# Kernel optimization log

Measured on AMD Instinct MI355X. Metric: run time of the kernel, lower is better.

Reference implementation:

```python
import jax, jax.numpy as jnp
import numpy as np

K = 3          # kernel size
K2 = K * K     # ope_channels


def setup_inputs() -> dict:
    key = jax.random.key(0)
    k1, k2, k3, k4, k5 = jax.random.split(key, 5)
    b, c, h, w = 8, 64, 128, 128
    out_c = 64
    x = jax.random.normal(k1, (b, c, h, w), dtype=jnp.float32)
    # conv weight: (in_channels, out_channels, k, k) as in the torch module
    weight = jax.random.normal(k2, (c, out_c, K, K), dtype=jnp.float32) * 0.05
    bias = jax.random.normal(k3, (out_c,), dtype=jnp.float32) * 0.05
    # operator MLP: Linear(K2 -> K2*K2); torch weight layout (out_features, in_features)
    op_w = jax.random.normal(k4, (K2 * K2, K2), dtype=jnp.float32) * 0.1
    op_b = jax.random.normal(k5, (K2 * K2,), dtype=jnp.float32) * 0.01
    return {"x": x, "weight": weight, "bias": bias, "op_w": op_w, "op_b": op_b}


def _unfold(x):
    # F.unfold(kernel=3, stride=1, pad=1) -> patches ordered (c, ki, kj)
    b, c, h, w = x.shape
    xp = jnp.pad(x, ((0, 0), (0, 0), (1, 1), (1, 1)))
    # (b, c, K2, h, w) with K2 ordered row-major over (ki, kj), matching torch
    patches = jnp.stack([xp[:, :, i:i + h, j:j + w]
                         for i in range(K) for j in range(K)], axis=2)
    return patches.transpose(0, 1, 3, 4, 2)  # (b, c, h, w, K2)


def reference(x, weight, bias, op_w, op_b):
    b, c, h, w = x.shape
    xu = _unfold(x)  # (b, c, h, w, K2)
    # per-pixel patch norm over channels -> (b, h, w, K2)
    n = jnp.sqrt(jnp.sum(xu * xu, axis=1))
    # per-pixel dynamic operator: (b, h, w, K2, K2)
    op = jnp.tanh(n @ op_w.T + op_b).reshape(b, h, w, K2, K2)
    # apply operator: bchw j , bhw jk -> bchw k
    x_op = jnp.einsum('bchwj,bhwjk->bchwk', xu, op)
    # final conv weight contraction: weight (in, out, K, K) -> (out, in, K2)
    wr = weight.reshape(c, -1, K2).transpose(1, 0, 2)
    out = jnp.einsum('bchwk,ock->bohw', x_op + xu, wr)
    return out + bias[None, :, None, None]
```

## Files before the change

### kernel.cpp

```cpp
#include <hip/hip_runtime.h>
#include <math.h>
#include <stdint.h>

#define HW   128
#define CIN  64
#define OC   64
#define TW   16
#define TH   4
#define HLW  18
#define HLH  6
#define HLN  (HLW*HLH)
#define SXR  109
#define K2   9
#define KTOT (CIN*K2)
#define SOPR 81

typedef __bf16  bf16x8 __attribute__((ext_vector_type(8)));
typedef float   f32x4  __attribute__((ext_vector_type(4)));
typedef uint32_t u32x4 __attribute__((ext_vector_type(4)));

__device__ __forceinline__ ushort f32_to_bf16_rne(float f) {
    union { float f; uint32_t u; } x; x.f = f;
    return (ushort)((x.u + 0x7FFF + ((x.u >> 16) & 1)) >> 16);
}

#define PKBF16(dst, lo, hi) \
    asm("v_cvt_pk_bf16_f32 %0, %1, %2" : "=v"(dst) : "v"(lo), "v"(hi))

__global__ void prep_weight(const float* __restrict__ w, ushort* __restrict__ wt) {
    int n = blockIdx.x * 256 + threadIdx.x;
    int o = n / KTOT;
    int r = n - o * KTOT;
    int kt = r >> 6;
    int c  = r & 63;
    wt[n] = f32_to_bf16_rne(w[(c * OC + o) * K2 + kt]);
}

__global__ __launch_bounds__(256, 2)
void dyf_main(const float* __restrict__ x,
              const float* __restrict__ bias,
              const float* __restrict__ op_w,
              const float* __restrict__ op_b,
              const ushort* __restrict__ wt,
              float* __restrict__ out)
{
    __shared__ float sx[CIN * SXR];
    __shared__ float sT[HLN];
    __shared__ float sop[64 * SOPR];

    const int tid  = threadIdx.x;
    const int lane = tid & 63;
    const int wv   = tid >> 6;
    const int b    = blockIdx.z;
    const int h0   = blockIdx.y * TH;
    const int w0   = blockIdx.x * TW;

    {
        const float* __restrict__ xb = x + (size_t)b * CIN * HW * HW;
        #pragma unroll
        for (int it = 0; it < 27; ++it) {
            int i  = tid + it * 256;
            int c  = i / HLN;
            int r  = i - c * HLN;
            int hy = r / HLW;
            int hx = r - hy * HLW;
            int gy = h0 - 1 + hy;
            int gx = w0 - 1 + hx;
            float v = 0.f;
            if ((unsigned)gy < HW && (unsigned)gx < HW)
                v = xb[c * HW * HW + gy * HW + gx];
            sx[c * SXR + r] = v;
        }
    }
    __syncthreads();

    if (tid < HLN) {
        float s = 0.f;
        #pragma unroll 16
        for (int c = 0; c < CIN; ++c) { float v = sx[c * SXR + tid]; s += v * v; }
        sT[tid] = s;
    }
    __syncthreads();

    {
        const int px = tid >> 2;
        const int q  = tid & 3;
        const int py = px >> 4, pxx = px & 15;
        float nrm[9];
        #pragma unroll
        for (int j = 0; j < 9; ++j)
            nrm[j] = sqrtf(sT[(py + j / 3) * HLW + pxx + (j % 3)]);
        const int nkt = (q == 0) ? 3 : 2;
        for (int t = 0; t < 3; ++t) {
            if (t >= nkt) break;
            const int kt = (q == 0) ? ((t == 2) ? 8 : t) : (q * 2 + t);
            #pragma unroll
            for (int j = 0; j < 9; ++j) {
                const int m = j * 9 + kt;
                float a = op_b[m];
                #pragma unroll
                for (int jj = 0; jj < 9; ++jj) a += nrm[jj] * op_w[m * 9 + jj];
                float v = tanhf(a);
                if (j == kt) v += 1.0f;
                sop[px * SOPR + m] = v;
            }
        }
    }
    __syncthreads();

    const int pxx = lane & 15;
    const int g   = lane >> 4;
    const int py  = wv;

    float opf[81];
    {
        const float* srcp = &sop[(wv * 16 + pxx) * SOPR];
        #pragma unroll
        for (int m = 0; m < 81; ++m) opf[m] = srcp[m];
    }

    u32x4 zw[18];
    #pragma unroll
    for (int chalf = 0; chalf < 2; ++chalf) {
        #pragma unroll
        for (int t = 0; t < 4; ++t) {
            const int c0 = chalf * 32 + g * 8 + 2 * t;
            float xu0[9], xu1[9];
            #pragma unroll
            for (int j = 0; j < 9; ++j) {
                const int pos = (py + j / 3) * HLW + pxx + (j % 3);
                xu0[j] = sx[c0 * SXR + pos];
                xu1[j] = sx[(c0 + 1) * SXR + pos];
            }
            #pragma unroll
            for (int kt = 0; kt < 9; ++kt) {
                float y0 = 0.f, y1 = 0.f;
                #pragma unroll
                for (int j = 0; j < 9; ++j) {
                    y0 += xu0[j] * opf[j * 9 + kt];
                    y1 += xu1[j] * opf[j * 9 + kt];
                }
                uint32_t pk;
                PKBF16(pk, y0, y1);
                zw[2 * kt + chalf][t] = pk;
            }
        }
    }

    __builtin_amdgcn_sched_barrier(0);

    {
        f32x4 acc[4];
        #pragma unroll
        for (int mr = 0; mr < 4; ++mr) acc[mr] = f32x4{0.f, 0.f, 0.f, 0.f};

        #pragma unroll
        for (int s = 0; s < 18; ++s) {
            const bf16x8 bfr = __builtin_bit_cast(bf16x8, zw[s]);
            #pragma unroll
            for (int mr = 0; mr < 4; ++mr) {
                const bf16x8 af = *reinterpret_cast<const bf16x8*>(
                    wt + (mr * 16 + pxx) * KTOT + s * 32 + g * 8);
                acc[mr] = __builtin_amdgcn_mfma_f32_16x16x32_bf16(af, bfr, acc[mr], 0, 0, 0);
            }
        }
        #pragma unroll
        for (int mr = 0; mr < 4; ++mr) {
            #pragma unroll
            for (int ii = 0; ii < 4; ++ii) {
                const int o = mr * 16 + g * 4 + ii;
                out[(((size_t)b * OC + o) * HW + (h0 + wv)) * HW + w0 + pxx]
                    = acc[mr][ii] + bias[o];
            }
        }
    }
}

extern "C" void kernel_launch(void* const* d_in, const int* in_sizes, int n_in,
                              void* d_out, int out_size, void* d_ws, size_t ws_size,
                              hipStream_t stream) {
    const float* x      = (const float*)d_in[0];
    const float* weight = (const float*)d_in[1];
    const float* bias   = (const float*)d_in[2];
    const float* op_w   = (const float*)d_in[3];
    const float* op_b   = (const float*)d_in[4];
    float*  out = (float*)d_out;
    ushort* wt  = (ushort*)d_ws;

    prep_weight<<<dim3((OC * KTOT) / 256), dim3(256), 0, stream>>>(weight, wt);

    dim3 grid(HW / TW, HW / TH, 8);
    dyf_main<<<grid, dim3(256), 0, stream>>>(x, bias, op_w, op_b, wt, out);
}
```

Before: 217.5 us.

## Pack per-pixel operator as bf16 and interleave MFMA per channel half

The 81-entry per-pixel operator is now stored in shared memory and registers as packed bf16 pairs, transposed by output tap, instead of fp32. The MFMA accumulation is split into two halves interleaved with the operator application, so only 9 packed fragments are live at once instead of 18. Together these cut register pressure enough to raise launch bounds from 2 to 3 blocks per SIMD set and shrink LDS use. The cost is extra bf16 rounding of the dynamic operator and unpack ALU work inside the inner loop.

New measurement: 236.5 us. 1.09x slower.

```diff
diff --git a/kernel.cpp b/kernel.cpp
--- a/kernel.cpp
+++ b/kernel.cpp
@@ -13,7 +13,7 @@
 #define SXR  109
 #define K2   9
 #define KTOT (CIN*K2)
-#define SOPR 81
+#define SOPW 54
 
 typedef __bf16  bf16x8 __attribute__((ext_vector_type(8)));
 typedef float   f32x4  __attribute__((ext_vector_type(4)));
@@ -23,6 +23,8 @@
     union { float f; uint32_t u; } x; x.f = f;
     return (ushort)((x.u + 0x7FFF + ((x.u >> 16) & 1)) >> 16);
 }
+__device__ __forceinline__ float bflo(uint32_t w) { return __uint_as_float(w << 16); }
+__device__ __forceinline__ float bfhi(uint32_t w) { return __uint_as_float(w & 0xffff0000u); }
 
 #define PKBF16(dst, lo, hi) \
     asm("v_cvt_pk_bf16_f32 %0, %1, %2" : "=v"(dst) : "v"(lo), "v"(hi))
@@ -36,7 +38,7 @@
     wt[n] = f32_to_bf16_rne(w[(c * OC + o) * K2 + kt]);
 }
 
-__global__ __launch_bounds__(256, 2)
+__global__ __launch_bounds__(256, 3)
 void dyf_main(const float* __restrict__ x,
               const float* __restrict__ bias,
               const float* __restrict__ op_w,
@@ -44,9 +46,9 @@
               const ushort* __restrict__ wt,
               float* __restrict__ out)
 {
-    __shared__ float sx[CIN * SXR];
-    __shared__ float sT[HLN];
-    __shared__ float sop[64 * SOPR];
+    __shared__ float    sx[CIN * SXR];
+    __shared__ float    sT[HLN];
+    __shared__ uint32_t sopp[64 * SOPW];
 
     const int tid  = threadIdx.x;
     const int lane = tid & 63;
@@ -94,16 +96,25 @@
         for (int t = 0; t < 3; ++t) {
             if (t >= nkt) break;
             const int kt = (q == 0) ? ((t == 2) ? 8 : t) : (q * 2 + t);
+            float tv[9];
             #pragma unroll
             for (int j = 0; j < 9; ++j) {
                 const int m = j * 9 + kt;
                 float a = op_b[m];
                 #pragma unroll
                 for (int jj = 0; jj < 9; ++jj) a += nrm[jj] * op_w[m * 9 + jj];
-                float v = tanhf(a);
-                if (j == kt) v += 1.0f;
-                sop[px * SOPR + m] = v;
-            }
+                tv[j] = tanhf(a);
+            }
+            tv[kt] += 1.0f;
+            const float fz = 0.0f;
+            uint32_t pw0, pw1, pw2, pw3, pw4;
+            PKBF16(pw0, tv[0], tv[1]);
+            PKBF16(pw1, tv[2], tv[3]);
+            PKBF16(pw2, tv[4], tv[5]);
+            PKBF16(pw3, tv[6], tv[7]);
+            PKBF16(pw4, tv[8], fz);
+            uint32_t* d = &sopp[px * SOPW + kt * 6];
+            d[0] = pw0; d[1] = pw1; d[2] = pw2; d[3] = pw3; d[4] = pw4;
         }
     }
     __syncthreads();
@@ -112,16 +123,26 @@
     const int g   = lane >> 4;
     const int py  = wv;
 
-    float opf[81];
+    uint32_t ow[45];
     {
-        const float* srcp = &sop[(wv * 16 + pxx) * SOPR];
-        #pragma unroll
-        for (int m = 0; m < 81; ++m) opf[m] = srcp[m];
-    }
-
-    u32x4 zw[18];
+        const uint32_t* srcp = &sopp[(wv * 16 + pxx) * SOPW];
+        #pragma unroll
+        for (int kt = 0; kt < 9; ++kt) {
+            uint2 a = *reinterpret_cast<const uint2*>(srcp + kt * 6);
+            uint2 c = *reinterpret_cast<const uint2*>(srcp + kt * 6 + 2);
+            ow[kt * 5 + 0] = a.x; ow[kt * 5 + 1] = a.y;
+            ow[kt * 5 + 2] = c.x; ow[kt * 5 + 3] = c.y;
+            ow[kt * 5 + 4] = srcp[kt * 6 + 4];
+        }
+    }
+
+    f32x4 acc[4];
+    #pragma unroll
+    for (int mr = 0; mr < 4; ++mr) acc[mr] = f32x4{0.f, 0.f, 0.f, 0.f};
+
     #pragma unroll
     for (int chalf = 0; chalf < 2; ++chalf) {
+        u32x4 zh[9];
         #pragma unroll
         for (int t = 0; t < 4; ++t) {
             const int c0 = chalf * 32 + g * 8 + 2 * t;
@@ -134,29 +155,27 @@
             }
             #pragma unroll
             for (int kt = 0; kt < 9; ++kt) {
+                float opv[9];
+                opv[0] = bflo(ow[kt*5+0]); opv[1] = bfhi(ow[kt*5+0]);
+                opv[2] = bflo(ow[kt*5+1]); opv[3] = bfhi(ow[kt*5+1]);
+                opv[4] = bflo(ow[kt*5+2]); opv[5] = bfhi(ow[kt*5+2]);
+                opv[6] = bflo(ow[kt*5+3]); opv[7] = bfhi(ow[kt*5+3]);
+                opv[8] = bflo(ow[kt*5+4]);
                 float y0 = 0.f, y1 = 0.f;
                 #pragma unroll
                 for (int j = 0; j < 9; ++j) {
-                    y0 += xu0[j] * opf[j * 9 + kt];
-                    y1 += xu1[j] * opf[j * 9 + kt];
+                    y0 += xu0[j] * opv[j];
+                    y1 += xu1[j] * opv[j];
                 }
                 uint32_t pk;
                 PKBF16(pk, y0, y1);
-                zw[2 * kt + chalf][t] = pk;
-            }
-        }
-    }
-
-    __builtin_amdgcn_sched_barrier(0);
-
-    {
-        f32x4 acc[4];
-        #pragma unroll
-        for (int mr = 0; mr < 4; ++mr) acc[mr] = f32x4{0.f, 0.f, 0.f, 0.f};
-
-        #pragma unroll
-        for (int s = 0; s < 18; ++s) {
-            const bf16x8 bfr = __builtin_bit_cast(bf16x8, zw[s]);
+                zh[kt][t] = pk;
+            }
+        }
+        #pragma unroll
+        for (int kt = 0; kt < 9; ++kt) {
+            const int s = 2 * kt + chalf;
+            const bf16x8 bfr = __builtin_bit_cast(bf16x8, zh[kt]);
             #pragma unroll
             for (int mr = 0; mr < 4; ++mr) {
                 const bf16x8 af = *reinterpret_cast<const bf16x8*>(
@@ -164,14 +183,15 @@
                 acc[mr] = __builtin_amdgcn_mfma_f32_16x16x32_bf16(af, bfr, acc[mr], 0, 0, 0);
             }
         }
-        #pragma unroll
-        for (int mr = 0; mr < 4; ++mr) {
-            #pragma unroll
-            for (int ii = 0; ii < 4; ++ii) {
-                const int o = mr * 16 + g * 4 + ii;
-                out[(((size_t)b * OC + o) * HW + (h0 + wv)) * HW + w0 + pxx]
-                    = acc[mr][ii] + bias[o];
-            }
+    }
+
+    #pragma unroll
+    for (int mr = 0; mr < 4; ++mr) {
+        #pragma unroll
+        for (int ii = 0; ii < 4; ++ii) {
+            const int o = mr * 16 + g * 4 + ii;
+            out[(((size_t)b * OC + o) * HW + (h0 + wv)) * HW + w0 + pxx]
+                = acc[mr][ii] + bias[o];
         }
     }
 }
```
